# Performance work log

Measured on AMD Instinct MI355X. Metric: run time of the kernel, lower is better.

The kernel has to match this reference:

```python
import jax, jax.numpy as jnp
import numpy as np

EPS = 1e-12   # F.normalize default eps
TH = 0.5      # forward-arg default threshold
CLAMP_LO, CLAMP_HI = 0.01, 0.999


def setup_inputs() -> dict:
    key = jax.random.key(0)
    k1, k2 = jax.random.split(key)
    # x4: ResNet layer3 features after ala1 scaling + upfeat, stride-16 of a 1024px image
    x4 = jax.random.normal(k1, (8, 1024, 64, 64), dtype=jnp.float32)
    # logits: classifier output after upfeat, same spatial grid, 21 classes
    logits = jax.random.normal(k2, (8, 21, 64, 64), dtype=jnp.float32)
    return {"x4": x4, "logits": logits, "pcm": 2}


def reference(x4, logits, pcm):
    b, c, h, w = x4.shape
    hw = h * w
    xf = x4.reshape(b, c, hw)                      # [b, c, hw]
    # F.normalize(dim=1): x / max(||x||_2, eps)
    norm = jnp.sqrt(jnp.sum(xf * xf, axis=1, keepdims=True))
    xn = xf / jnp.maximum(norm, EPS)
    # pixel affinity: [b, hw, hw]
    aff = jnp.einsum('bci,bcj->bij', xn, xn)
    aff = jnp.clip(aff, CLAMP_LO, CLAMP_HI)
    aff = jnp.where(aff < TH, jnp.zeros((), aff.dtype), aff)
    # column-normalize (torch sum over dim=1)
    aff = aff / jnp.sum(aff, axis=1, keepdims=True)
    lf = logits.reshape(b, -1, hw)                 # [b, K, hw]
    for _ in range(pcm):                           # pcm is a Python int
        lf = jnp.einsum('bki,bij->bkj', lf, aff)
    return lf.reshape(b, -1, h, w)
```

## Files before the change

### kernel.cpp

```cpp
#include <hip/hip_runtime.h>
#include <hip/hip_bf16.h>

#define B_  8
#define C_  1024
#define HW_ 4096
#define NK  21
#define NT  32
#define NTRI (NT * (NT + 1) / 2)

using bf16 = __hip_bfloat16;
typedef __attribute__((ext_vector_type(4))) float float4_;
typedef __attribute__((ext_vector_type(2))) long long2_;

__global__ __launch_bounds__(256) void knorm1(const float* __restrict__ x4, float* __restrict__ sumsq) {
    int t = threadIdx.x;
    int b = blockIdx.z;
    int c0 = blockIdx.y * 128;
    int j = blockIdx.x * 256 + t;
    const float* p = x4 + ((size_t)b * C_ + c0) * HW_ + j;
    float s = 0.f;
#pragma unroll 8
    for (int c = 0; c < 128; ++c) {
        float v = p[(size_t)c * HW_];
        s = fmaf(v, v, s);
    }
    atomicAdd(&sumsq[b * HW_ + j], s);
}

__global__ __launch_bounds__(256) void ktrans(const float* __restrict__ x4, const float* __restrict__ sumsq,
                                              unsigned char* __restrict__ Xn8) {
    int b = blockIdx.z, ct = blockIdx.y, jt = blockIdx.x;
    int c0 = ct * 128, j0 = jt * 64;
    int t = threadIdx.x;
    __shared__ float tile[128][65];

    int jl = t & 63, cl = t >> 6;
#pragma unroll
    for (int cc = 0; cc < 128; cc += 4)
        tile[cc + cl][jl] = x4[((size_t)b * C_ + c0 + cc + cl) * HW_ + j0 + jl];
    __syncthreads();

    int j = t >> 2, q = t & 3;
    int jg = j0 + j;
    float inv = 1.0f / fmaxf(sqrtf(sumsq[b * HW_ + jg]), 1e-12f);

#pragma unroll
    for (int pass = 0; pass < 2; ++pass) {
        int u = pass * 4 + q;
        int p = u >> 2, lk = u & 3;
        unsigned int pk[4];
#pragma unroll
        for (int h = 0; h < 2; ++h) {
            int kbase = (2 * p + h) * 32 + lk * 8;
#pragma unroll
            for (int g = 0; g < 2; ++g) {
                float f0 = tile[kbase + g * 4 + 0][j] * inv;
                float f1 = tile[kbase + g * 4 + 1][j] * inv;
                float f2 = tile[kbase + g * 4 + 2][j] * inv;
                float f3 = tile[kbase + g * 4 + 3][j] * inv;
                unsigned int r = 0;
                r = __builtin_amdgcn_cvt_pk_fp8_f32(f0, f1, r, false);
                r = __builtin_amdgcn_cvt_pk_fp8_f32(f2, f3, r, true);
                pk[h * 2 + g] = r;
            }
        }
        *(uint4*)(Xn8 + ((size_t)b * HW_ + jg) * C_ + c0 + u * 16) =
            make_uint4(pk[0], pk[1], pk[2], pk[3]);
    }
}

__global__ __launch_bounds__(256) void kgram(const unsigned char* __restrict__ Xn8, bf16* __restrict__ aff,
                                             float* __restrict__ colsum, int* __restrict__ flags) {
    int b = blockIdx.y;
    int p = blockIdx.x;
    int it = (int)((2.0f * NT + 1.0f - sqrtf((2.0f * NT + 1.0f) * (2.0f * NT + 1.0f) - 8.0f * (float)p)) * 0.5f);
    while (it > 0 && p < it * NT - it * (it - 1) / 2) --it;
    while (p >= (it + 1) * NT - (it + 1) * it / 2) ++it;
    int jt = it + p - (it * NT - it * (it - 1) / 2);

    int i0 = it * 128, j0 = jt * 128;
    int t = threadIdx.x, w = t >> 6, l = t & 63;
    int wr = w >> 1, wc = w & 1;
    int lrow = l & 15, lk = l >> 4;

    __shared__ __align__(16) unsigned char As[128 * 128];
    __shared__ __align__(16) unsigned char Bs[128 * 128];
    __shared__ int fl;

    const unsigned char* XA = Xn8 + ((size_t)b * HW_ + i0) * C_;
    const unsigned char* XB = Xn8 + ((size_t)b * HW_ + j0) * C_;

    int srow = l >> 3;
    int sslot = l & 7;

    float4_ acc[4][4];
#pragma unroll
    for (int m = 0; m < 4; ++m)
#pragma unroll
        for (int n = 0; n < 4; ++n) acc[m][n] = {0.f, 0.f, 0.f, 0.f};

    for (int k0 = 0; k0 < C_; k0 += 128) {
        __syncthreads();
#pragma unroll
        for (int q = 0; q < 4; ++q) {
            int R = (w * 4 + q) * 8 + srow;
            int gp = sslot ^ (R & 7);
            __builtin_amdgcn_global_load_lds(
                (const __attribute__((address_space(1))) void*)(XA + (size_t)R * C_ + k0 + gp * 16),
                (__attribute__((address_space(3))) void*)(As + R * 128 + sslot * 16), 16, 0, 0);
            __builtin_amdgcn_global_load_lds(
                (const __attribute__((address_space(1))) void*)(XB + (size_t)R * C_ + k0 + gp * 16),
                (__attribute__((address_space(3))) void*)(Bs + R * 128 + sslot * 16), 16, 0, 0);
        }
        __syncthreads();
#pragma unroll
        for (int pp = 0; pp < 2; ++pp) {
            long2_ av[4], bv[4];
#pragma unroll
            for (int m = 0; m < 4; ++m) {
                int r = wr * 64 + m * 16 + lrow;
                av[m] = *(const long2_*)(As + r * 128 + ((pp * 4 + lk) ^ (r & 7)) * 16);
            }
#pragma unroll
            for (int n = 0; n < 4; ++n) {
                int r = wc * 64 + n * 16 + lrow;
                bv[n] = *(const long2_*)(Bs + r * 128 + ((pp * 4 + lk) ^ (r & 7)) * 16);
            }
#pragma unroll
            for (int m = 0; m < 4; ++m)
#pragma unroll
                for (int n = 0; n < 4; ++n) {
                    acc[m][n] = __builtin_amdgcn_mfma_f32_16x16x32_fp8_fp8(av[m].x, bv[n].x, acc[m][n], 0, 0, 0);
                    acc[m][n] = __builtin_amdgcn_mfma_f32_16x16x32_fp8_fp8(av[m].y, bv[n].y, acc[m][n], 0, 0, 0);
                }
        }
    }

    bool any = false;
#pragma unroll
    for (int m = 0; m < 4; ++m)
#pragma unroll
        for (int n = 0; n < 4; ++n)
#pragma unroll
            for (int r = 0; r < 4; ++r) any |= (acc[m][n][r] >= 0.5f);

    if (t == 0) fl = 0;
    __syncthreads();
    unsigned long long bal = __ballot(any);
    if (l == 0 && bal != 0ull) atomicOr(&fl, 1);
    __syncthreads();
    bool mirror = (it != jt);
    if (t == 0) {
        flags[(b * NT + it) * NT + jt] = fl;
        if (mirror) flags[(b * NT + jt) * NT + it] = fl;
    }

    if (fl) {
        size_t affb = (size_t)b * HW_ * HW_;
        float rsum[4][4];
#pragma unroll
        for (int m = 0; m < 4; ++m)
#pragma unroll
            for (int r = 0; r < 4; ++r) rsum[m][r] = 0.f;

#pragma unroll
        for (int n = 0; n < 4; ++n) {
            int j = j0 + wc * 64 + n * 16 + lrow;
            float cs = 0.f;
#pragma unroll
            for (int m = 0; m < 4; ++m) {
#pragma unroll
                for (int r = 0; r < 4; ++r) {
                    float v = acc[m][n][r];
                    v = fminf(fmaxf(v, 0.01f), 0.999f);
                    v = (v < 0.5f) ? 0.0f : v;
                    bf16 bb = __float2bfloat16(v);
                    int i = i0 + wr * 64 + m * 16 + lk * 4 + r;
                    aff[affb + (size_t)i * HW_ + j] = bb;
                    float bf = __bfloat162float(bb);
                    cs += bf;
                    rsum[m][r] += bf;
                    if (mirror) aff[affb + (size_t)j * HW_ + i] = bb;
                }
            }
            cs += __shfl_xor(cs, 16);
            cs += __shfl_xor(cs, 32);
            if (lk == 0) atomicAdd(&colsum[b * HW_ + j], cs);
        }
        if (mirror) {
#pragma unroll
            for (int m = 0; m < 4; ++m) {
#pragma unroll
                for (int r = 0; r < 4; ++r) {
                    float s = rsum[m][r];
                    s += __shfl_xor(s, 1);
                    s += __shfl_xor(s, 2);
                    s += __shfl_xor(s, 4);
                    s += __shfl_xor(s, 8);
                    if (lrow == 0) {
                        int i = i0 + wr * 64 + m * 16 + lk * 4 + r;
                        atomicAdd(&colsum[b * HW_ + i], s);
                    }
                }
            }
        }
    }
}

__global__ __launch_bounds__(128) void kprop(const float* __restrict__ lf, const bf16* __restrict__ aff,
                                             const int* __restrict__ flags, const float* __restrict__ colsum,
                                             float* __restrict__ outp) {
    int b = blockIdx.y, jt = blockIdx.x;
    int t = threadIdx.x;
    int j = jt * 128 + t;
    __shared__ float lfs[NK * 128];
    float acc[NK];
#pragma unroll
    for (int k = 0; k < NK; ++k) acc[k] = 0.f;

    for (int it = 0; it < NT; ++it) {
        if (flags[(b * NT + it) * NT + jt] == 0) continue;
        __syncthreads();
        for (int idx = t; idx < NK * 128; idx += 128)
            lfs[idx] = lf[((size_t)b * NK + (idx >> 7)) * HW_ + it * 128 + (idx & 127)];
        __syncthreads();
        const bf16* ap = aff + ((size_t)b * HW_ + it * 128) * HW_ + j;
        for (int ii = 0; ii < 128; ++ii) {
            float a = __bfloat162float(ap[(size_t)ii * HW_]);
#pragma unroll
            for (int k = 0; k < NK; ++k)
                acc[k] = fmaf(lfs[(k << 7) + ii], a, acc[k]);
        }
    }
    float inv = 1.0f / colsum[b * HW_ + j];
#pragma unroll
    for (int k = 0; k < NK; ++k)
        outp[((size_t)b * NK + k) * HW_ + j] = acc[k] * inv;
}

extern "C" void kernel_launch(void* const* d_in, const int* in_sizes, int n_in,
                              void* d_out, int out_size, void* d_ws, size_t ws_size,
                              hipStream_t stream) {
    const float* x4 = (const float*)d_in[0];
    const float* logits = (const float*)d_in[1];
    float* out = (float*)d_out;

    char* w = (char*)d_ws;
    size_t off = 0;
    auto take = [&](size_t bytes) {
        char* p = w + off;
        off += (bytes + 255) & ~(size_t)255;
        return p;
    };
    unsigned char* Xn8 = (unsigned char*)take((size_t)B_ * HW_ * C_);
    bf16* aff     = (bf16*)take((size_t)B_ * HW_ * HW_ * 2);
    float* colsum = (float*)take((size_t)B_ * HW_ * 4);
    int*   flags  = (int*)take((size_t)B_ * NT * NT * 4);
    float* sumsq  = (float*)take((size_t)B_ * HW_ * 4);
    float* lf1    = (float*)take((size_t)B_ * NK * HW_ * 4);

    hipMemsetAsync(colsum, 0, (size_t)B_ * HW_ * 4 + (size_t)B_ * NT * NT * 4 + (size_t)B_ * HW_ * 4, stream);

    knorm1<<<dim3(HW_ / 256, 8, B_), dim3(256), 0, stream>>>(x4, sumsq);
    ktrans<<<dim3(HW_ / 64, C_ / 128, B_), dim3(256), 0, stream>>>(x4, sumsq, Xn8);
    kgram <<<dim3(NTRI, B_), dim3(256), 0, stream>>>(Xn8, aff, colsum, flags);

    kprop<<<dim3(NT, B_), dim3(128), 0, stream>>>(logits, aff, flags, colsum, lf1);
    kprop<<<dim3(NT, B_), dim3(128), 0, stream>>>(lf1, aff, flags, colsum, out);
}
```

Baseline: 367.7 us.

## Fuse norm pass into transpose, apply normalization post-GEMM, use 16x16x128 scaled fp8 MFMA

Removes the separate sum-of-squares kernel by accumulating squared norms inside the transpose/quantize kernel, and quantizes unnormalized features to fp8, scaling the Gram result by reciprocal row/column norms afterward. The GEMM inner loop switches from pairs of 16x16x32 fp8 MFMAs to a single MX-scaled 16x16x128 f8f6f4 MFMA per tile with unit scales. This saves one full read of x4 and reduces MFMA issue count. The cost is that raw values are quantized to fp8 without prior normalization, which changes rounding and range behaviour.

Result: faster. 355.2 us (-3.4%).

```diff
diff --git a/kernel.cpp b/kernel.cpp
--- a/kernel.cpp
+++ b/kernel.cpp
@@ -10,66 +10,52 @@
 
 using bf16 = __hip_bfloat16;
 typedef __attribute__((ext_vector_type(4))) float float4_;
-typedef __attribute__((ext_vector_type(2))) long long2_;
-
-__global__ __launch_bounds__(256) void knorm1(const float* __restrict__ x4, float* __restrict__ sumsq) {
-    int t = threadIdx.x;
-    int b = blockIdx.z;
-    int c0 = blockIdx.y * 128;
-    int j = blockIdx.x * 256 + t;
-    const float* p = x4 + ((size_t)b * C_ + c0) * HW_ + j;
-    float s = 0.f;
-#pragma unroll 8
-    for (int c = 0; c < 128; ++c) {
-        float v = p[(size_t)c * HW_];
-        s = fmaf(v, v, s);
-    }
-    atomicAdd(&sumsq[b * HW_ + j], s);
-}
-
-__global__ __launch_bounds__(256) void ktrans(const float* __restrict__ x4, const float* __restrict__ sumsq,
-                                              unsigned char* __restrict__ Xn8) {
+typedef __attribute__((ext_vector_type(8))) int int8v;
+
+__global__ __launch_bounds__(256) void ktrans(const float* __restrict__ x4, float* __restrict__ sumsq,
+                                              unsigned char* __restrict__ Xq) {
     int b = blockIdx.z, ct = blockIdx.y, jt = blockIdx.x;
     int c0 = ct * 128, j0 = jt * 64;
     int t = threadIdx.x;
     __shared__ float tile[128][65];
+    __shared__ float ssq[64];
 
     int jl = t & 63, cl = t >> 6;
-#pragma unroll
-    for (int cc = 0; cc < 128; cc += 4)
-        tile[cc + cl][jl] = x4[((size_t)b * C_ + c0 + cc + cl) * HW_ + j0 + jl];
+    if (t < 64) ssq[t] = 0.f;
+    __syncthreads();
+    float part = 0.f;
+#pragma unroll
+    for (int cc = 0; cc < 128; cc += 4) {
+        float v = x4[((size_t)b * C_ + c0 + cc + cl) * HW_ + j0 + jl];
+        tile[cc + cl][jl] = v;
+        part = fmaf(v, v, part);
+    }
+    atomicAdd(&ssq[jl], part);
     __syncthreads();
 
     int j = t >> 2, q = t & 3;
     int jg = j0 + j;
-    float inv = 1.0f / fmaxf(sqrtf(sumsq[b * HW_ + jg]), 1e-12f);
-
-#pragma unroll
-    for (int pass = 0; pass < 2; ++pass) {
-        int u = pass * 4 + q;
-        int p = u >> 2, lk = u & 3;
-        unsigned int pk[4];
-#pragma unroll
-        for (int h = 0; h < 2; ++h) {
-            int kbase = (2 * p + h) * 32 + lk * 8;
-#pragma unroll
-            for (int g = 0; g < 2; ++g) {
-                float f0 = tile[kbase + g * 4 + 0][j] * inv;
-                float f1 = tile[kbase + g * 4 + 1][j] * inv;
-                float f2 = tile[kbase + g * 4 + 2][j] * inv;
-                float f3 = tile[kbase + g * 4 + 3][j] * inv;
-                unsigned int r = 0;
-                r = __builtin_amdgcn_cvt_pk_fp8_f32(f0, f1, r, false);
-                r = __builtin_amdgcn_cvt_pk_fp8_f32(f2, f3, r, true);
-                pk[h * 2 + g] = r;
-            }
-        }
-        *(uint4*)(Xn8 + ((size_t)b * HW_ + jg) * C_ + c0 + u * 16) =
-            make_uint4(pk[0], pk[1], pk[2], pk[3]);
-    }
-}
-
-__global__ __launch_bounds__(256) void kgram(const unsigned char* __restrict__ Xn8, bf16* __restrict__ aff,
+    unsigned int pk[8];
+#pragma unroll
+    for (int g = 0; g < 8; ++g) {
+        float f0 = tile[q * 32 + g * 4 + 0][j];
+        float f1 = tile[q * 32 + g * 4 + 1][j];
+        float f2 = tile[q * 32 + g * 4 + 2][j];
+        float f3 = tile[q * 32 + g * 4 + 3][j];
+        unsigned int r = 0;
+        r = __builtin_amdgcn_cvt_pk_fp8_f32(f0, f1, r, false);
+        r = __builtin_amdgcn_cvt_pk_fp8_f32(f2, f3, r, true);
+        pk[g] = r;
+    }
+    unsigned char* dst = Xq + ((size_t)b * HW_ + jg) * C_ + c0 + q * 32;
+    *(uint4*)(dst)      = make_uint4(pk[0], pk[1], pk[2], pk[3]);
+    *(uint4*)(dst + 16) = make_uint4(pk[4], pk[5], pk[6], pk[7]);
+
+    if (t < 64) atomicAdd(&sumsq[b * HW_ + j0 + t], ssq[t]);
+}
+
+__global__ __launch_bounds__(256) void kgram(const unsigned char* __restrict__ Xq,
+                                             const float* __restrict__ sumsq, bf16* __restrict__ aff,
                                              float* __restrict__ colsum, int* __restrict__ flags) {
     int b = blockIdx.y;
     int p = blockIdx.x;
@@ -87,8 +73,8 @@
     __shared__ __align__(16) unsigned char Bs[128 * 128];
     __shared__ int fl;
 
-    const unsigned char* XA = Xn8 + ((size_t)b * HW_ + i0) * C_;
-    const unsigned char* XB = Xn8 + ((size_t)b * HW_ + j0) * C_;
+    const unsigned char* XA = Xq + ((size_t)b * HW_ + i0) * C_;
+    const unsigned char* XB = Xq + ((size_t)b * HW_ + j0) * C_;
 
     int srow = l >> 3;
     int sslot = l & 7;
@@ -113,28 +99,54 @@
                 (__attribute__((address_space(3))) void*)(Bs + R * 128 + sslot * 16), 16, 0, 0);
         }
         __syncthreads();
-#pragma unroll
-        for (int pp = 0; pp < 2; ++pp) {
-            long2_ av[4], bv[4];
-#pragma unroll
-            for (int m = 0; m < 4; ++m) {
-                int r = wr * 64 + m * 16 + lrow;
-                av[m] = *(const long2_*)(As + r * 128 + ((pp * 4 + lk) ^ (r & 7)) * 16);
-            }
-#pragma unroll
-            for (int n = 0; n < 4; ++n) {
-                int r = wc * 64 + n * 16 + lrow;
-                bv[n] = *(const long2_*)(Bs + r * 128 + ((pp * 4 + lk) ^ (r & 7)) * 16);
-            }
-#pragma unroll
-            for (int m = 0; m < 4; ++m)
-#pragma unroll
-                for (int n = 0; n < 4; ++n) {
-                    acc[m][n] = __builtin_amdgcn_mfma_f32_16x16x32_fp8_fp8(av[m].x, bv[n].x, acc[m][n], 0, 0, 0);
-                    acc[m][n] = __builtin_amdgcn_mfma_f32_16x16x32_fp8_fp8(av[m].y, bv[n].y, acc[m][n], 0, 0, 0);
-                }
-        }
-    }
+
+        int8v av[4], bv[4];
+#pragma unroll
+        for (int m = 0; m < 4; ++m) {
+            int r = wr * 64 + m * 16 + lrow;
+            uint4 lo = *(const uint4*)(As + r * 128 + (((lk * 2) ^ (r & 7)) * 16));
+            uint4 hi = *(const uint4*)(As + r * 128 + (((lk * 2 + 1) ^ (r & 7)) * 16));
+            int8v v; v[0] = lo.x; v[1] = lo.y; v[2] = lo.z; v[3] = lo.w;
+            v[4] = hi.x; v[5] = hi.y; v[6] = hi.z; v[7] = hi.w;
+            av[m] = v;
+        }
+#pragma unroll
+        for (int n = 0; n < 4; ++n) {
+            int r = wc * 64 + n * 16 + lrow;
+            uint4 lo = *(const uint4*)(Bs + r * 128 + (((lk * 2) ^ (r & 7)) * 16));
+            uint4 hi = *(const uint4*)(Bs + r * 128 + (((lk * 2 + 1) ^ (r & 7)) * 16));
+            int8v v; v[0] = lo.x; v[1] = lo.y; v[2] = lo.z; v[3] = lo.w;
+            v[4] = hi.x; v[5] = hi.y; v[6] = hi.z; v[7] = hi.w;
+            bv[n] = v;
+        }
+#pragma unroll
+        for (int m = 0; m < 4; ++m)
+#pragma unroll
+            for (int n = 0; n < 4; ++n)
+                acc[m][n] = __builtin_amdgcn_mfma_scale_f32_16x16x128_f8f6f4(
+                    av[m], bv[n], acc[m][n], 0, 0, 0, 0x7f7f7f7f, 0, 0x7f7f7f7f);
+    }
+
+    float rnj[4], rni[4][4];
+#pragma unroll
+    for (int n = 0; n < 4; ++n) {
+        int j = j0 + wc * 64 + n * 16 + lrow;
+        rnj[n] = 1.0f / fmaxf(sqrtf(sumsq[b * HW_ + j]), 1e-12f);
+    }
+#pragma unroll
+    for (int m = 0; m < 4; ++m)
+#pragma unroll
+        for (int r = 0; r < 4; ++r) {
+            int i = i0 + wr * 64 + m * 16 + lk * 4 + r;
+            rni[m][r] = 1.0f / fmaxf(sqrtf(sumsq[b * HW_ + i]), 1e-12f);
+        }
+#pragma unroll
+    for (int m = 0; m < 4; ++m)
+#pragma unroll
+        for (int n = 0; n < 4; ++n)
+#pragma unroll
+            for (int r = 0; r < 4; ++r)
+                acc[m][n][r] *= rni[m][r] * rnj[n];
 
     bool any = false;
 #pragma unroll
@@ -252,7 +264,7 @@
         off += (bytes + 255) & ~(size_t)255;
         return p;
     };
-    unsigned char* Xn8 = (unsigned char*)take((size_t)B_ * HW_ * C_);
+    unsigned char* Xq = (unsigned char*)take((size_t)B_ * HW_ * C_);
     bf16* aff     = (bf16*)take((size_t)B_ * HW_ * HW_ * 2);
     float* colsum = (float*)take((size_t)B_ * HW_ * 4);
     int*   flags  = (int*)take((size_t)B_ * NT * NT * 4);
@@ -261,9 +273,8 @@
 
     hipMemsetAsync(colsum, 0, (size_t)B_ * HW_ * 4 + (size_t)B_ * NT * NT * 4 + (size_t)B_ * HW_ * 4, stream);
 
-    knorm1<<<dim3(HW_ / 256, 8, B_), dim3(256), 0, stream>>>(x4, sumsq);
-    ktrans<<<dim3(HW_ / 64, C_ / 128, B_), dim3(256), 0, stream>>>(x4, sumsq, Xn8);
-    kgram <<<dim3(NTRI, B_), dim3(256), 0, stream>>>(Xn8, aff, colsum, flags);
+    ktrans<<<dim3(HW_ / 64, C_ / 128, B_), dim3(256), 0, stream>>>(x4, sumsq, Xq);
+    kgram <<<dim3(NTRI, B_), dim3(256), 0, stream>>>(Xq, sumsq, aff, colsum, flags);
 
     kprop<<<dim3(NT, B_), dim3(128), 0, stream>>>(logits, aff, flags, colsum, lf1);
     kprop<<<dim3(NT, B_), dim3(128), 0, stream>>>(lf1, aff, flags, colsum, out);
```
